# Kernel tuning notes

Measured on AMD Instinct MI355X. Metric: run time of the kernel, lower is better.

Reference implementation:

```python
import jax, jax.numpy as jnp
import numpy as np


def leaky(x):
    return jnp.where(x > 0, x, 0.2 * x)


def conv(x, w, b, s, p):
    y = jax.lax.conv_general_dilated(x, w, (s, s), [(p, p), (p, p)],
                                     dimension_numbers=('NCHW', 'OIHW', 'NCHW'))
    return y + b[None, :, None, None]


def maxpool2s1(x):
    return jax.lax.reduce_window(x, -jnp.inf, jax.lax.max, (1, 1, 2, 2), (1, 1, 1, 1), 'VALID')


def bn_eval(x, g, b, m, v):
    scale = g / jnp.sqrt(v + 1e-5)
    return (x - m[None, :, None, None]) * scale[None, :, None, None] + b[None, :, None, None]


def adaptive_avg_pool(x, oh, ow):
    # matches torch AdaptiveAvgPool2d window rule: [floor(i*H/o), ceil((i+1)*H/o))
    B, C, H, W = x.shape
    rows = []
    for i in range(oh):
        hs, he = (i * H) // oh, -((-(i + 1) * H) // oh)
        cols = []
        for j in range(ow):
            ws, we = (j * W) // ow, -((-(j + 1) * W) // ow)
            cols.append(x[:, :, hs:he, ws:we].mean((2, 3)))
        rows.append(jnp.stack(cols, -1))
    return jnp.stack(rows, -2)  # [B,C,oh,ow]


def forward(x, tw1, tb1, tw2, tb2, tw3, tb3, tw4, tb4,
            sw1, sb1, bn1_g, bn1_b, bn1_m, bn1_v,
            sw2, sb2, bn2_g, bn2_b, bn2_m, bn2_v,
            cw, cb, ew1, eb1, ew2, eb2, ew3, eb3):
    B = x.shape[0]
    E, K = ew1.shape[0], 2
    # --- scout router (BN in eval mode with running stats) ---
    h = jax.nn.relu(bn_eval(conv(x, sw1, sb1, 4, 3), bn1_g, bn1_b, bn1_m, bn1_v))
    h = jax.nn.relu(bn_eval(conv(h, sw2, sb2, 2, 1), bn2_g, bn2_b, bn2_m, bn2_v))
    logits = h.mean((2, 3)) @ cw.T + cb                       # [B,E]
    gate = jax.nn.softmax(logits, axis=-1)
    topk_p, topk_i = jax.lax.top_k(gate, K)                   # [B,K]
    topk_p = topk_p / (topk_p.sum(-1, keepdims=True) + 1e-6)
    # --- shared trunk ---
    t = maxpool2s1(leaky(conv(x, tw1, tb1, 4, 1)))            # 224->56->55
    t = maxpool2s1(leaky(conv(t, tw2, tb2, 2, 2)))            # 55->28->27
    t = leaky(conv(t, tw3, tb3, 1, 1))                        # 27
    t = maxpool2s1(leaky(conv(t, tw4, tb4, 1, 1)))            # 27->26
    t = adaptive_avg_pool(t, 3, 3)                            # [B,128,3,3]
    flat = t.reshape(B, -1)                                   # [B,1152]
    # --- MoE head: dense per-expert MLP, masked weighted combine ---
    h1 = leaky(jnp.einsum('bi,eoi->beo', flat, ew1) + eb1[None])   # [B,E,1024]
    h2 = leaky(jnp.einsum('beh,eoh->beo', h1, ew2) + eb2[None])    # [B,E,512]
    h3 = jnp.einsum('beh,eoh->beo', h2, ew3) + eb3[None]           # [B,E,feat]
    onehot = (topk_i[:, :, None] == jnp.arange(E)[None, None, :])  # [B,K,E]
    comb_w = jnp.sum(topk_p[:, :, None] * onehot, axis=1)          # [B,E]
    out = jnp.einsum('beo,be->bo', h3, comb_w)                     # [B,feat]
    return out


def setup_inputs() -> dict:
    key = jax.random.key(0)
    ks = jax.random.split(key, 32)
    W = 0.02
    d = {}
    d['x'] = jax.random.normal(ks[0], (256, 3, 224, 224), jnp.float32)
    d['tw1'] = jax.random.normal(ks[1], (16, 3, 3, 3), jnp.float32) * W
    d['tb1'] = jnp.zeros((16,), jnp.float32)
    d['tw2'] = jax.random.normal(ks[2], (32, 16, 5, 5), jnp.float32) * W
    d['tb2'] = jnp.zeros((32,), jnp.float32)
    d['tw3'] = jax.random.normal(ks[3], (64, 32, 3, 3), jnp.float32) * W
    d['tb3'] = jnp.zeros((64,), jnp.float32)
    d['tw4'] = jax.random.normal(ks[4], (128, 64, 3, 3), jnp.float32) * W
    d['tb4'] = jnp.zeros((128,), jnp.float32)
    d['sw1'] = jax.random.normal(ks[5], (16, 3, 7, 7), jnp.float32) * W
    d['sb1'] = jnp.zeros((16,), jnp.float32)
    d['bn1_g'] = jnp.ones((16,), jnp.float32)
    d['bn1_b'] = jnp.zeros((16,), jnp.float32)
    d['bn1_m'] = jnp.zeros((16,), jnp.float32)
    d['bn1_v'] = jnp.ones((16,), jnp.float32)
    d['sw2'] = jax.random.normal(ks[6], (32, 16, 3, 3), jnp.float32) * W
    d['sb2'] = jnp.zeros((32,), jnp.float32)
    d['bn2_g'] = jnp.ones((32,), jnp.float32)
    d['bn2_b'] = jnp.zeros((32,), jnp.float32)
    d['bn2_m'] = jnp.zeros((32,), jnp.float32)
    d['bn2_v'] = jnp.ones((32,), jnp.float32)
    d['cw'] = jax.random.normal(ks[7], (3, 32), jnp.float32) * W
    d['cb'] = jnp.zeros((3,), jnp.float32)
    d['ew1'] = jax.random.normal(ks[8], (3, 1024, 1152), jnp.float32) * W
    d['eb1'] = jnp.zeros((3, 1024), jnp.float32)
    d['ew2'] = jax.random.normal(ks[9], (3, 512, 1024), jnp.float32) * W
    d['eb2'] = jnp.zeros((3, 512), jnp.float32)
    d['ew3'] = jax.random.normal(ks[10], (3, 512, 512), jnp.float32) * W
    d['eb3'] = jnp.zeros((3, 512), jnp.float32)
    return d


def reference(x, tw1, tb1, tw2, tb2, tw3, tb3, tw4, tb4,
              sw1, sb1, bn1_g, bn1_b, bn1_m, bn1_v,
              sw2, sb2, bn2_g, bn2_b, bn2_m, bn2_v,
              cw, cb, ew1, eb1, ew2, eb2, ew3, eb3):
    return forward(x, tw1, tb1, tw2, tb2, tw3, tb3, tw4, tb4,
                   sw1, sb1, bn1_g, bn1_b, bn1_m, bn1_v,
                   sw2, sb2, bn2_g, bn2_b, bn2_m, bn2_v,
                   cw, cb, ew1, eb1, ew2, eb2, ew3, eb3)
```

## Files before the change

### kernel.cpp

```cpp
#include <hip/hip_runtime.h>

#define DEV static __device__ __forceinline__

constexpr int BATCH = 256;

DEV float leakyf(float x){ return x > 0.f ? x : 0.2f * x; }

typedef _Float16 f16x8 __attribute__((ext_vector_type(8)));
typedef float f32x4 __attribute__((ext_vector_type(4)));

DEV f16x8 max8(f16x8 a, f16x8 b){
  f16x8 r;
  #pragma unroll
  for (int j = 0; j < 8; ++j) r[j] = a[j] > b[j] ? a[j] : b[j];
  return r;
}

template<int IC,int OC>
DEV void wpackM_body(int i, const float* __restrict__ w, _Float16* __restrict__ wp){
  constexpr int F = OC/16;
  int j = i & 7, L = (i >> 3) & 63, rest = i >> 9;
  int f = rest % F; int q2 = rest / F; int s = q2 % (IC/32); int t = q2 / (IC/32);
  int oc = f*16 + (L & 15), ic = s*32 + (L >> 4)*8 + j;
  wp[i] = (_Float16)w[((size_t)oc*IC + ic)*9 + t];
}

template<int OC,int K>
DEV void wpackS_body(int i, const float* __restrict__ w, _Float16* __restrict__ wp){
  constexpr int F = OC/16, KWP = (K+1)/2;
  int j = i & 7, L = (i >> 3) & 63, rest = i >> 9;
  int f = rest % F, s = rest / F;
  int kh = s / KWP, kwp = s % KWP;
  int k = (L >> 4)*8 + j;
  int kw = 2*kwp + (k >> 4), ic = k & 15;
  int oc = f*16 + (L & 15);
  float v = (kw < K) ? w[((size_t)(oc*16 + ic)*K + kh)*K + kw] : 0.f;
  wp[i] = (_Float16)v;
}

DEV void wpackF_body(int i, const float* __restrict__ sw1,
                     const float* __restrict__ tw1, _Float16* __restrict__ wp){
  int j = i & 7, L = (i >> 3) & 63, rest = i >> 9;
  int nf = rest & 1, s = rest >> 1;
  int k = s*32 + (L >> 4)*8 + j;
  int oc = L & 15;
  int t = k / 48, c = k % 48;
  int dr = (t >> 1) - 1, dc = (t & 1) - 1;
  int ic = c >> 4, pr = (c >> 2) & 3, pc = c & 3;
  float v = 0.f;
  if (nf == 0){
    int kh = 4*dr + pr + 3, kw = 4*dc + pc + 3;
    if (kh >= 0 && kh < 7 && kw >= 0 && kw < 7) v = sw1[((oc*3 + ic)*7 + kh)*7 + kw];
  } else {
    int kh = 4*dr + pr + 1, kw = 4*dc + pc + 1;
    if (kh >= 0 && kh < 3 && kw >= 0 && kw < 3) v = tw1[((oc*3 + ic)*3 + kh)*3 + kw];
  }
  wp[i] = (_Float16)v;
}

template<int KTOT>
DEV void wpackG_body(int i, int e, const float* __restrict__ w, int N,
                     _Float16* __restrict__ wp){
  const int NF = N >> 4;
  const int total = NF * (KTOT >> 5) * 512;
  w  += (size_t)e * N * KTOT;
  wp += (size_t)e * total;
  int j = i & 7, L = (i >> 3) & 63, rest = i >> 9;
  int nf = rest % NF, t = rest / NF;
  int n = nf*16 + (L & 15), k = t*32 + (L >> 4)*8 + j;
  wp[i] = (_Float16)w[(size_t)n*KTOT + k];
}

__global__ __launch_bounds__(256) void wpackC_k(
    const float* __restrict__ tw3, _Float16* __restrict__ wpk3,
    const float* __restrict__ tw4, _Float16* __restrict__ wpk4,
    const float* __restrict__ tw2, _Float16* __restrict__ wp2,
    const float* __restrict__ sw2, _Float16* __restrict__ wps2,
    const float* __restrict__ sw1, const float* __restrict__ tw1,
    _Float16* __restrict__ wpf, float* __restrict__ gsum){
  const int b = blockIdx.x;
  const int tid = threadIdx.x;
  if (b < 72){
    wpackM_body<32,64>(b*256 + tid, tw3, wpk3);
  } else if (b < 360){
    wpackM_body<64,128>((b-72)*256 + tid, tw4, wpk4);
  } else if (b < 420){
    wpackS_body<32,5>((b-360)*256 + tid, tw2, wp2);
  } else if (b < 444){
    wpackS_body<32,3>((b-420)*256 + tid, sw2, wps2);
  } else if (b < 468){
    wpackF_body((b-444)*256 + tid, sw1, tw1, wpf);
  } else {
    gsum[(b-468)*256 + tid] = 0.f;
  }
}

__global__ __launch_bounds__(256) void fusedX_k(
    const float* __restrict__ x,
    const _Float16* __restrict__ W,
    const float* __restrict__ sb, const float* __restrict__ cb_,
    const float* __restrict__ g, const float* __restrict__ bt,
    const float* __restrict__ mn, const float* __restrict__ vr,
    _Float16* __restrict__ s1out, _Float16* __restrict__ c1out,
    const float* __restrict__ ew1, _Float16* __restrict__ ewp1,
    const float* __restrict__ ew2, _Float16* __restrict__ ewp2,
    const float* __restrict__ ew3, _Float16* __restrict__ ewp3){
  __shared__ __align__(16) _Float16 Ah[3*58*64];
  const int tid = threadIdx.x;
  const int b = blockIdx.x;

  if (b < 23040){
    if (b < 13824){
      wpackG_body<1152>((b % 4608)*256 + tid, b / 4608, ew1, 1024, ewp1);
    } else if (b < 19968){
      int t2 = b - 13824;
      wpackG_body<1024>((t2 % 2048)*256 + tid, t2 / 2048, ew2, 512, ewp2);
    } else {
      int t3 = b - 19968;
      wpackG_body<512>((t3 % 1024)*256 + tid, t3 / 1024, ew3, 512, ewp3);
    }
    return;
  }

  const int lb = b - 23040;
  const int w = (lb & 7)*896 + (lb >> 3);
  const int n = w / 28, oh0 = (w % 28) * 2;

  if (tid < 48){
    int rr = tid >> 4, side = (tid >> 3) & 1, q = tid & 7;
    int col = side ? 57 : 0;
    *(int4*)((char*)Ah + (((rr*58 + col) << 7) + q*16)) = (int4){0,0,0,0};
  }

  {
    const int m = tid & 63;
    const bool mok = (m < 56);
    const int mc = mok ? m : 55;
    const int cc = m + 1;
    const int rc0 = tid >> 6;

    float4 vv[9];
    {
      int ic   = (rc0 == 3) ? 0 : rc0;
      int ridx = (rc0 == 3) ? 1 : 0;
      #pragma unroll
      for (int j = 0; j < 9; ++j){
        const int ih = 4*oh0 - 4 + ridx;
        const int ihc = ih < 0 ? 0 : ih;
        const float* p = x + ((size_t)(n*3 + ic)*224 + ihc)*224 + 4*mc;
        asm volatile("global_load_dwordx4 %0, %1, off"
                     : "=v"(vv[j]) : "v"(p));
        ic += 1; ridx += 1;
        if (ic >= 3){ ic -= 3; ridx += 1; }
      }
    }
    asm volatile("s_waitcnt vmcnt(0)" ::: "memory");
    __builtin_amdgcn_sched_barrier(0);
    if (mok){
      int ic   = (rc0 == 3) ? 0 : rc0;
      int ridx = (rc0 == 3) ? 1 : 0;
      #pragma unroll
      for (int j = 0; j < 9; ++j){
        const int ih = 4*oh0 - 4 + ridx;
        float4 v = (ih >= 0) ? vv[j] : (float4){0.f,0.f,0.f,0.f};
        const int rr = ridx >> 2, pr = ridx & 3;
        int boff = (((rr*58 + cc) << 7) + ic*32 + pr*8) ^ ((cc & 7) << 4);
        _Float16 h4[4] = {(_Float16)v.x, (_Float16)v.y,
                          (_Float16)v.z, (_Float16)v.w};
        *(unsigned long long*)((char*)Ah + boff) = *(unsigned long long*)h4;
        ic += 1; ridx += 1;
        if (ic >= 3){ ic -= 3; ridx += 1; }
      }
    }
  }
  __syncthreads();

  const int wid = tid >> 6, lane = tid & 63;
  const int kg8 = (lane >> 4) * 8;
  f32x4 acc[2][2];
  #pragma unroll
  for (int mi = 0; mi < 2; ++mi)
    #pragma unroll
    for (int nf = 0; nf < 2; ++nf) acc[mi][nf] = (f32x4){0.f,0.f,0.f,0.f};

  #pragma unroll
  for (int s = 0; s < 6; ++s){
    const int kk = s*32 + kg8;
    const int t = kk / 48, c0 = kk - t*48;
    const int ra = t >> 1, ca = t & 1;
    f16x8 ah[2];
    #pragma unroll
    for (int mi = 0; mi < 2; ++mi){
      const int m = 2*wid + mi;
      const int rowsel = m >> 2;
      const int ow = (m & 3)*16 + (lane & 15);
      const int owc = ow > 55 ? 55 : ow;
      const int col = owc + ca;
      const int bidx = ((((rowsel + ra)*58 + col) << 7) + c0*2) ^ ((col & 7) << 4);
      ah[mi] = *(const f16x8*)((const char*)Ah + bidx);
    }
    #pragma unroll
    for (int nf = 0; nf < 2; ++nf){
      const f16x8 bw = *(const f16x8*)(W + (s*2 + nf)*512 + lane*8);
      #pragma unroll
      for (int mi = 0; mi < 2; ++mi)
        acc[mi][nf] = __builtin_amdgcn_mfma_f32_16x16x32_f16(ah[mi], bw, acc[mi][nf], 0,0,0);
    }
  }

  const int oc = lane & 15;
  const float sbv = sb[oc];
  const float scv = g[oc] * __frsqrt_rn(vr[oc] + 1e-5f);
  const float mnv = mn[oc], btv = bt[oc], cbv = cb_[oc];
  #pragma unroll
  for (int mi = 0; mi < 2; ++mi){
    const int m = 2*wid + mi;
    const int row = oh0 + (m >> 2);
    const int owb = (m & 3)*16 + (lane >> 4)*4;
    #pragma unroll
    for (int r = 0; r < 4; ++r){
      const int ow = owb + r;
      if (ow >= 56) continue;
      float vs = acc[mi][0][r] + sbv;
      vs = fmaxf((vs - mnv)*scv + btv, 0.f);
      const size_t o = (((size_t)n*56 + row)*56 + ow)*16 + oc;
      s1out[o] = (_Float16)vs;
      c1out[o] = (_Float16)leakyf(acc[mi][1][r] + cbv);
    }
  }
}

template<int OC,int K,int P,int IH,int IW,int ACT,bool OUT16,bool GATE,bool POOLIN>
DEV void convS_body(int bx, int tid, _Float16* A, float* gred,
    const _Float16* __restrict__ in,
    const _Float16* __restrict__ W,
    const float* __restrict__ bias,
    const float* __restrict__ bng, const float* __restrict__ bnb,
    const float* __restrict__ bnm, const float* __restrict__ bnv,
    float* __restrict__ outF, _Float16* __restrict__ outH,
    float* __restrict__ gsum){
  constexpr int F = OC/16, KWP = (K+1)/2;
  constexpr int RW = POOLIN ? (IW+1) : IW;

  const int n = bx / 28, oh = bx % 28;

  if (GATE && tid < 32) gred[tid] = 0.f;

  for (int i = tid; i < K*60*2; i += 256){
    int half = i & 1; int p = i >> 1;
    int c = p % 60; int r = p / 60;
    int ih = 2*oh - P + r, iw = c - P;
    int4 v = {0,0,0,0};
    if (ih >= 0 && ih < IH && iw >= 0 && iw < IW){
      const _Float16* q = in + (((size_t)n*(POOLIN ? IH+1 : IH) + ih)*RW + iw)*16 + half*8;
      if (POOLIN){
        f16x8 a = *(const f16x8*)q;
        f16x8 b = *(const f16x8*)(q + 16);
        f16x8 cc = *(const f16x8*)(q + RW*16);
        f16x8 d = *(const f16x8*)(q + RW*16 + 16);
        f16x8 mx = max8(max8(a, b), max8(cc, d));
        v = *(int4*)&mx;
      } else {
        v = *(const int4*)q;
      }
    }
    int byte = ((r*60 + c)*32 + half*16) ^ (((c>>1)&7) << 4);
    *(int4*)((char*)A + byte) = v;
  }
  __syncthreads();

  const int wid = tid >> 6, lane = tid & 63;
  const int fsel = wid & 1, mb = wid >> 1;
  const int ow_l = min(mb*16 + (lane & 15), 27);
  const int ic0b = ((lane >> 4) & 1) * 16;
  const int kwo  = (lane >> 4) >> 1;

  f32x4 acc = {0.f,0.f,0.f,0.f};
  #pragma unroll
  for (int kh = 0; kh < K; ++kh){
    #pragma unroll
    for (int kwp = 0; kwp < KWP; ++kwp){
      const int kw = 2*kwp + kwo;
      const int c = 2*ow_l + kw;
      int byte = ((kh*60 + c)*32 + ic0b) ^ (((c>>1)&7) << 4);
      f16x8 a = *(const f16x8*)((const char*)A + byte);
      const int s = kh*KWP + kwp;
      const f16x8 b = *(const f16x8*)(W + (s*F + fsel)*512 + lane*8);
      acc = __builtin_amdgcn_mfma_f32_16x16x32_f16(a, b, acc, 0,0,0);
    }
  }

  const int oc = fsel*16 + (lane & 15);
  float bv = bias[oc], sc = 1.f, mm = 0.f, bb = 0.f;
  if (ACT == 1){
    sc = bng[oc] * __frsqrt_rn(bnv[oc] + 1e-5f);
    mm = bnm[oc]; bb = bnb[oc];
  }
  float lsum = 0.f;
  #pragma unroll
  for (int r = 0; r < 4; ++r){
    const int ow = mb*16 + (lane >> 4)*4 + r;
    if (ow >= 28) continue;
    float v = acc[r] + bv;
    if (ACT == 1) v = fmaxf((v - mm)*sc + bb, 0.f);
    else          v = leakyf(v);
    if (GATE){
      lsum += v;
    } else {
      const size_t o = (((size_t)n*28 + oh)*28 + ow)*OC + oc;
      if (OUT16) outH[o] = (_Float16)v;
      else       outF[o] = v;
    }
  }
  if (GATE){
    atomicAdd(&gred[oc], lsum);
    __syncthreads();
    if (tid < 32) atomicAdd(&gsum[n*32 + tid], gred[tid]);
  }
}

__global__ __launch_bounds__(256) void convSS_k(
    const _Float16* __restrict__ s1h, const _Float16* __restrict__ wps2,
    const float* __restrict__ sb2,
    const float* __restrict__ bn2g, const float* __restrict__ bn2b,
    const float* __restrict__ bn2m, const float* __restrict__ bn2v,
    float* __restrict__ gsum,
    const _Float16* __restrict__ c1h, const _Float16* __restrict__ wp2,
    const float* __restrict__ tb2, _Float16* __restrict__ c2h){
  __shared__ __align__(16) _Float16 A[5*60*16];
  __shared__ float gred[32];
  const int tid = threadIdx.x;
  if (blockIdx.x < BATCH*28){
    convS_body<32,3,1,56,56,1,false,true,false>(blockIdx.x, tid, A, gred,
        s1h, wps2, sb2, bn2g, bn2b, bn2m, bn2v, nullptr, nullptr, gsum);
  } else {
    convS_body<32,5,2,55,55,0,true,false,true>(blockIdx.x - BATCH*28, tid, A, gred,
        c1h, wp2, tb2, nullptr, nullptr, nullptr, nullptr, nullptr, c2h, nullptr);
  }
}

template<int IC,int OC,bool POOLIN>
__global__ __launch_bounds__(256) void convM_k(
    const _Float16* __restrict__ Ag,
    const _Float16* __restrict__ W,
    const float* __restrict__ bias,
    _Float16* __restrict__ Out)
{
  constexpr int S = IC/32, FTOT = OC/16, FW = FTOT/2;
  constexpr int ICB = IC*2, ICG = ICB/16;
  __shared__ __align__(16) char A[4*34*ICB];

  const int tid = threadIdx.x;
  const int bx = blockIdx.x;
  const int n = bx / 14, pr = bx % 14;
  const int oh0 = pr * 2;

  for (int g = tid; g < 4*34*ICG; g += 256){
    int r = g / (34*ICG);
    int rem = g - r*(34*ICG);
    int c = rem / ICG, q = rem - c*ICG;
    int ir = oh0 + r - 1, icol = c - 1;
    int4 v = {0,0,0,0};
    if (ir >= 0 && ir < 27 && icol >= 0 && icol < 27){
      if (POOLIN){
        const _Float16* p0 = Ag + (((size_t)n*28 + ir)*28 + icol)*IC + q*8;
        f16x8 a = *(const f16x8*)p0;
        f16x8 b = *(const f16x8*)(p0 + IC);
        f16x8 cc = *(const f16x8*)(p0 + 28*IC);
        f16x8 d = *(const f16x8*)(p0 + 28*IC + IC);
        f16x8 mx = max8(max8(a, b), max8(cc, d));
        v = *(int4*)&mx;
      } else {
        v = *(const int4*)(Ag + (((size_t)n*27 + ir)*27 + icol)*IC + q*8);
      }
    }
    int off = (r*34 + c)*ICB + q*16;
    int swz = off ^ ((c & 7) << 4);
    *(int4*)(A + swz) = v;
  }
  __syncthreads();

  const int wid = tid >> 6, lane = tid & 63;
  const int rsel = wid & 1, ocq = wid >> 1;
  const int c0 = lane & 15, kg = (lane >> 4) * 16;
  const int colb0 = c0*ICB + kg, colb1 = (16 + c0)*ICB + kg;
  int msk[3];
  #pragma unroll
  for (int kw = 0; kw < 3; ++kw) msk[kw] = ((c0 + kw) & 7) << 4;

  f32x4 acc[2][FW];
  #pragma unroll
  for (int m = 0; m < 2; ++m)
    #pragma unroll
    for (int f = 0; f < FW; ++f) acc[m][f] = (f32x4){0.f,0.f,0.f,0.f};

  #pragma unroll
  for (int kh = 0; kh < 3; ++kh){
    #pragma unroll
    for (int kw = 0; kw < 3; ++kw){
      #pragma unroll
      for (int s = 0; s < S; ++s){
        const int fr0 = (((kh*3 + kw)*S + s)*FTOT + ocq*FW) * 512 + lane*8;
        f16x8 b[FW];
        #pragma unroll
        for (int f = 0; f < FW; ++f)
          b[f] = *(const f16x8*)(W + fr0 + f*512);
        const int base = ((rsel + kh)*34 + kw)*ICB + s*64;
        const int o0 = (base + colb0) ^ msk[kw];
        const int o1 = (base + colb1) ^ msk[kw];
        f16x8 a0 = *(const f16x8*)(A + o0);
        f16x8 a1 = *(const f16x8*)(A + o1);
        #pragma unroll
        for (int f = 0; f < FW; ++f){
          acc[0][f] = __builtin_amdgcn_mfma_f32_16x16x32_f16(a0, b[f], acc[0][f], 0,0,0);
          acc[1][f] = __builtin_amdgcn_mfma_f32_16x16x32_f16(a1, b[f], acc[1][f], 0,0,0);
        }
      }
    }
  }

  const int orow = oh0 + rsel;
  if (orow >= 27) return;
  #pragma unroll
  for (int f = 0; f < FW; ++f){
    const int oc = (ocq*FW + f)*16 + c0;
    const float bv = bias[oc];
    #pragma unroll
    for (int m = 0; m < 2; ++m){
      #pragma unroll
      for (int r = 0; r < 4; ++r){
        const int ow = m*16 + (lane >> 4)*4 + r;
        if (ow >= 27) continue;
        float v = leakyf(acc[m][f][r] + bv);
        Out[(((size_t)n*27 + orow)*27 + ow)*OC + oc] = (_Float16)v;
      }
    }
  }
}

template<int KTOT,int ACT>
__global__ __launch_bounds__(256) void gemmH_k(
    const _Float16* __restrict__ A, long strideA,
    const _Float16* __restrict__ W,
    const float* __restrict__ bias, int N,
    _Float16* __restrict__ OutH){
  const int e = blockIdx.z;
  A += (size_t)e * strideA;
  const int NF = N >> 4, KT = KTOT >> 5;
  W += (size_t)e * NF * KT * 512;
  const float* bs = bias + (size_t)e * N;
  const size_t ob = (size_t)e * 256 * N;

  const int tid = threadIdx.x, wid = tid >> 6, lane = tid & 63;
  const int mblk = blockIdx.x * 32;
  const int nf = blockIdx.y * 4 + wid;
  const int r0 = mblk + (lane & 15);
  const int kof = (lane >> 4) * 8;

  f32x4 acc0 = {0,0,0,0}, acc1 = {0,0,0,0};
  for (int t = 0; t < KT; ++t){
    const int k = t*32 + kof;
    f16x8 a0 = *(const f16x8*)(A + (size_t)r0*KTOT + k);
    f16x8 a1 = *(const f16x8*)(A + (size_t)(r0+16)*KTOT + k);
    const f16x8 b = *(const f16x8*)(W + ((size_t)t*NF + nf)*512 + lane*8);
    acc0 = __builtin_amdgcn_mfma_f32_16x16x32_f16(a0, b, acc0, 0,0,0);
    acc1 = __builtin_amdgcn_mfma_f32_16x16x32_f16(a1, b, acc1, 0,0,0);
  }
  const int n = nf*16 + (lane & 15);
  const float bv = bs[n];
  #pragma unroll
  for (int mi = 0; mi < 2; ++mi){
    f32x4 a = mi ? acc1 : acc0;
    #pragma unroll
    for (int r = 0; r < 4; ++r){
      const int m = mblk + mi*16 + (lane >> 4)*4 + r;
      float v = a[r] + bv;
      if (ACT == 1) v = leakyf(v);
      OutH[ob + (size_t)m*N + n] = (_Float16)v;
    }
  }
}

__global__ __launch_bounds__(256) void gemmC_k(
    const _Float16* __restrict__ A,
    const _Float16* __restrict__ W,
    const float* __restrict__ b3,
    const float* __restrict__ gsum,
    const float* __restrict__ cw, const float* __restrict__ cb,
    float* __restrict__ out){
  __shared__ float combL[16][3];
  const int tid = threadIdx.x, wid = tid >> 6, lane = tid & 63;
  const int mblk = blockIdx.x * 16;

  if (tid < 16){
    const int n = mblk + tid;
    float mch[32];
    #pragma unroll
    for (int c = 0; c < 32; ++c) mch[c] = gsum[n*32 + c] / 784.f;
    float lg[3];
    #pragma unroll
    for (int e = 0; e < 3; ++e){
      float a = cb[e];
      #pragma unroll
      for (int c = 0; c < 32; ++c) a += mch[c] * cw[e*32 + c];
      lg[e] = a;
    }
    float m = fmaxf(lg[0], fmaxf(lg[1], lg[2]));
    float ex[3], sum = 0.f;
    #pragma unroll
    for (int e = 0; e < 3; ++e){ ex[e] = expf(lg[e] - m); sum += ex[e]; }
    float pr[3];
    #pragma unroll
    for (int e = 0; e < 3; ++e) pr[e] = ex[e] / sum;
    int i1 = 0;
    if (pr[1] > pr[0]) i1 = 1;
    if (pr[2] > pr[i1]) i1 = 2;
    int i2 = -1;
    for (int e = 0; e < 3; ++e){
      if (e == i1) continue;
      if (i2 < 0 || pr[e] > pr[i2]) i2 = e;
    }
    float s12 = pr[i1] + pr[i2] + 1e-6f;
    float cmb[3] = {0.f, 0.f, 0.f};
    cmb[i1] = pr[i1] / s12;
    cmb[i2] = pr[i2] / s12;
    combL[tid][0] = cmb[0];
    combL[tid][1] = cmb[1];
    combL[tid][2] = cmb[2];
  }
  __syncthreads();

  const int nf = blockIdx.y * 4 + wid;
  const int r0 = mblk + (lane & 15);
  const int kof = (lane >> 4) * 8;
  const int n = nf*16 + (lane & 15);

  f32x4 oacc = {0.f,0.f,0.f,0.f};
  #pragma unroll
  for (int e = 0; e < 3; ++e){
    const _Float16* Ae = A + (size_t)e * 256 * 512;
    const _Float16* We = W + (size_t)e * 32 * 16 * 512;
    f32x4 acc = {0.f,0.f,0.f,0.f};
    for (int t = 0; t < 16; ++t){
      f16x8 a = *(const f16x8*)(Ae + (size_t)r0*512 + t*32 + kof);
      const f16x8 b = *(const f16x8*)(We + ((size_t)t*32 + nf)*512 + lane*8);
      acc = __builtin_amdgcn_mfma_f32_16x16x32_f16(a, b, acc, 0,0,0);
    }
    const float bv = b3[e*512 + n];
    #pragma unroll
    for (int r = 0; r < 4; ++r){
      const int lr = (lane >> 4)*4 + r;
      oacc[r] += combL[lr][e] * (acc[r] + bv);
    }
  }
  #pragma unroll
  for (int r = 0; r < 4; ++r){
    const int m = mblk + (lane >> 4)*4 + r;
    out[(size_t)m*512 + n] = oacc[r];
  }
}

__global__ __launch_bounds__(256) void papool2_k(const _Float16* __restrict__ in,
                                                 _Float16* __restrict__ flat16){
  __shared__ float red[2][128][9];
  const int n = blockIdx.x;
  const int tid = threadIdx.x;
  const int h = tid >> 7, c = tid & 127;
  const _Float16* p = in + (size_t)n * 729 * 128 + c;

  float sum[9];
  #pragma unroll
  for (int j = 0; j < 9; ++j) sum[j] = 0.f;

  float prev[27], cur[27];
  const int r0 = h * 13;
  #pragma unroll
  for (int rr = 0; rr < 14; ++rr){
    const int r = r0 + rr;
    #pragma unroll
    for (int cc = 0; cc < 27; ++cc)
      cur[cc] = (float)p[(size_t)(r*27 + cc) * 128];
    if (rr > 0){
      const int pr = r - 1;
      const bool b0 = (pr < 9), b1 = (pr >= 8) && (pr < 18), b2 = (pr >= 17);
      #pragma unroll
      for (int cc = 0; cc < 26; ++cc){
        float v = fmaxf(fmaxf(prev[cc], prev[cc+1]), fmaxf(cur[cc], cur[cc+1]));
        if (b0){
          if (cc < 9)             sum[0] += v;
          if (cc >= 8 && cc < 18) sum[1] += v;
          if (cc >= 17)           sum[2] += v;
        }
        if (b1){
          if (cc < 9)             sum[3] += v;
          if (cc >= 8 && cc < 18) sum[4] += v;
          if (cc >= 17)           sum[5] += v;
        }
        if (b2){
          if (cc < 9)             sum[6] += v;
          if (cc >= 8 && cc < 18) sum[7] += v;
          if (cc >= 17)           sum[8] += v;
        }
      }
    }
    #pragma unroll
    for (int cc = 0; cc < 27; ++cc) prev[cc] = cur[cc];
  }

  #pragma unroll
  for (int j = 0; j < 9; ++j) red[h][c][j] = sum[j];
  __syncthreads();

  if (tid < 128){
    const float rcp[9] = {1.f/81, 1.f/90, 1.f/81, 1.f/90, 1.f/100, 1.f/90,
                          1.f/81, 1.f/90, 1.f/81};
    _Float16* o = flat16 + (size_t)n * 1152 + tid * 9;
    #pragma unroll
    for (int j = 0; j < 9; ++j)
      o[j] = (_Float16)((red[0][tid][j] + red[1][tid][j]) * rcp[j]);
  }
}

extern "C" void kernel_launch(void* const* d_in, const int* in_sizes, int n_in,
                              void* d_out, int out_size, void* d_ws, size_t ws_size,
                              hipStream_t stream){
  const float* x    = (const float*)d_in[0];
  const float* tw1  = (const float*)d_in[1];  const float* tb1 = (const float*)d_in[2];
  const float* tw2  = (const float*)d_in[3];  const float* tb2 = (const float*)d_in[4];
  const float* tw3  = (const float*)d_in[5];  const float* tb3 = (const float*)d_in[6];
  const float* tw4  = (const float*)d_in[7];  const float* tb4 = (const float*)d_in[8];
  const float* sw1  = (const float*)d_in[9];  const float* sb1 = (const float*)d_in[10];
  const float* bn1g = (const float*)d_in[11]; const float* bn1b = (const float*)d_in[12];
  const float* bn1m = (const float*)d_in[13]; const float* bn1v = (const float*)d_in[14];
  const float* sw2  = (const float*)d_in[15]; const float* sb2 = (const float*)d_in[16];
  const float* bn2g = (const float*)d_in[17]; const float* bn2b = (const float*)d_in[18];
  const float* bn2m = (const float*)d_in[19]; const float* bn2v = (const float*)d_in[20];
  const float* cw   = (const float*)d_in[21]; const float* cb  = (const float*)d_in[22];
  const float* ew1  = (const float*)d_in[23]; const float* eb1 = (const float*)d_in[24];
  const float* ew2  = (const float*)d_in[25]; const float* eb2 = (const float*)d_in[26];
  const float* ew3  = (const float*)d_in[27]; const float* eb3 = (const float*)d_in[28];
  float* out = (float*)d_out;

  float* ws = (float*)d_ws;
  size_t off = 0;
  _Float16* flat16 = (_Float16*)(ws + off); off += 147456;
  float* gsum   = ws + off; off += BATCH * 32;
  _Float16* wpk3 = (_Float16*)(ws + off); off += 9216;
  _Float16* wpk4 = (_Float16*)(ws + off); off += 36864;
  _Float16* wp2  = (_Float16*)(ws + off); off += 7680;
  _Float16* wps2 = (_Float16*)(ws + off); off += 3072;
  _Float16* wpf  = (_Float16*)(ws + off); off += 3072;
  off += 16;
  float* bufA   = ws + off; off += 13778944;
  off += 16;
  float* bufB   = ws + off; off += 23887872;
  off += 16;
  (void)ws_size; (void)in_sizes; (void)n_in; (void)out_size;

  _Float16* s1h = (_Float16*)bufA;
  _Float16* C3u = (_Float16*)bufA;
  _Float16* ewp1 = (_Float16*)(bufA + 6500000);
  _Float16* ewp2 = ewp1 + 3538944;
  _Float16* ewp3 = ewp2 + 1572864;
  _Float16* c1h = (_Float16*)bufB;
  _Float16* c2h = (_Float16*)(bufB + 14000000);
  _Float16* c4h = (_Float16*)bufB;
  _Float16* h1  = (_Float16*)bufB;
  _Float16* h2  = h1 + 786432;

  dim3 blk(256);

  wpackC_k<<<dim3(500), blk, 0, stream>>>(
      tw3, wpk3, tw4, wpk4, tw2, wp2, sw2, wps2, sw1, tw1, wpf, gsum);

  fusedX_k<<<dim3(30208), blk, 0, stream>>>(
      x, wpf, sb1, tb1, bn1g, bn1b, bn1m, bn1v, s1h, c1h,
      ew1, ewp1, ew2, ewp2, ew3, ewp3);

  convSS_k<<<dim3(BATCH*28*2), blk, 0, stream>>>(
      s1h, wps2, sb2, bn2g, bn2b, bn2m, bn2v, gsum,
      c1h, wp2, tb2, c2h);

  convM_k<32,64,true><<<dim3(BATCH*14), blk, 0, stream>>>(
      c2h, wpk3, tb3, C3u);

  convM_k<64,128,false><<<dim3(BATCH*14), blk, 0, stream>>>(
      C3u, wpk4, tb4, c4h);

  papool2_k<<<dim3(BATCH), blk, 0, stream>>>(c4h, flat16);

  gemmH_k<1152,1><<<dim3(8,16,3), blk, 0, stream>>>(
      flat16, 0L, ewp1, eb1, 1024, h1);
  gemmH_k<1024,1><<<dim3(8,8,3), blk, 0, stream>>>(
      h1, 256L*1024, ewp2, eb2, 512, h2);
  gemmC_k<<<dim3(16,8), blk, 0, stream>>>(
      h2, ewp3, eb3, gsum, cw, cb, out);
}
```

Measured before the change: 244.7 us.

## Process four output rows per block in fused first conv with ring-buffered input

Each block of the fused first-layer conv now produces four output rows instead of two. It reuses the shared input row that overlaps between the two row pairs through a three-slot ring buffer in LDS. Loads for the second pair's new input rows are issued before the first pair's MFMA compute, which overlaps global latency with compute, and the conv grid shrinks by half. This cuts redundant input reads and per-block setup, at the cost of more registers held across compute, extra barriers, and fewer blocks for occupancy.

```diff
diff --git a/kernel.cpp b/kernel.cpp
--- a/kernel.cpp
+++ b/kernel.cpp
@@ -123,8 +123,8 @@
   }
 
   const int lb = b - 23040;
-  const int w = (lb & 7)*896 + (lb >> 3);
-  const int n = w / 28, oh0 = (w % 28) * 2;
+  const int w = (lb & 7)*448 + (lb >> 3);
+  const int n = w / 14, oh0 = (w % 14) * 4;
 
   if (tid < 48){
     int rr = tid >> 4, side = (tid >> 3) & 1, q = tid & 7;
@@ -132,13 +132,13 @@
     *(int4*)((char*)Ah + (((rr*58 + col) << 7) + q*16)) = (int4){0,0,0,0};
   }
 
+  const int m = tid & 63;
+  const bool mok = (m < 56);
+  const int mc = mok ? m : 55;
+  const int cc = m + 1;
+  const int rc0 = tid >> 6;
+
   {
-    const int m = tid & 63;
-    const bool mok = (m < 56);
-    const int mc = mok ? m : 55;
-    const int cc = m + 1;
-    const int rc0 = tid >> 6;
-
     float4 vv[9];
     {
       int ic   = (rc0 == 3) ? 0 : rc0;
@@ -175,59 +175,100 @@
   }
   __syncthreads();
 
+  float4 uu[6];
+  #pragma unroll
+  for (int j2 = 0; j2 < 6; ++j2){
+    const int k = rc0*6 + j2;
+    const int icn = k >> 3, nr = k & 7;
+    const int rrl = 1 + (nr >> 2), prn = nr & 3;
+    const int ih = 4*(oh0 + 1 + rrl) + prn;
+    const float* p = x + ((size_t)(n*3 + icn)*224 + ih)*224 + 4*mc;
+    asm volatile("global_load_dwordx4 %0, %1, off"
+                 : "=v"(uu[j2]) : "v"(p));
+  }
+
   const int wid = tid >> 6, lane = tid & 63;
   const int kg8 = (lane >> 4) * 8;
-  f32x4 acc[2][2];
-  #pragma unroll
-  for (int mi = 0; mi < 2; ++mi)
-    #pragma unroll
-    for (int nf = 0; nf < 2; ++nf) acc[mi][nf] = (f32x4){0.f,0.f,0.f,0.f};
-
-  #pragma unroll
-  for (int s = 0; s < 6; ++s){
-    const int kk = s*32 + kg8;
-    const int t = kk / 48, c0 = kk - t*48;
-    const int ra = t >> 1, ca = t & 1;
-    f16x8 ah[2];
-    #pragma unroll
-    for (int mi = 0; mi < 2; ++mi){
-      const int m = 2*wid + mi;
-      const int rowsel = m >> 2;
-      const int ow = (m & 3)*16 + (lane & 15);
-      const int owc = ow > 55 ? 55 : ow;
-      const int col = owc + ca;
-      const int bidx = ((((rowsel + ra)*58 + col) << 7) + c0*2) ^ ((col & 7) << 4);
-      ah[mi] = *(const f16x8*)((const char*)Ah + bidx);
-    }
-    #pragma unroll
-    for (int nf = 0; nf < 2; ++nf){
-      const f16x8 bw = *(const f16x8*)(W + (s*2 + nf)*512 + lane*8);
-      #pragma unroll
-      for (int mi = 0; mi < 2; ++mi)
-        acc[mi][nf] = __builtin_amdgcn_mfma_f32_16x16x32_f16(ah[mi], bw, acc[mi][nf], 0,0,0);
-    }
-  }
-
   const int oc = lane & 15;
   const float sbv = sb[oc];
   const float scv = g[oc] * __frsqrt_rn(vr[oc] + 1e-5f);
   const float mnv = mn[oc], btv = bt[oc], cbv = cb_[oc];
-  #pragma unroll
-  for (int mi = 0; mi < 2; ++mi){
-    const int m = 2*wid + mi;
-    const int row = oh0 + (m >> 2);
-    const int owb = (m & 3)*16 + (lane >> 4)*4;
-    #pragma unroll
-    for (int r = 0; r < 4; ++r){
-      const int ow = owb + r;
-      if (ow >= 56) continue;
-      float vs = acc[mi][0][r] + sbv;
-      vs = fmaxf((vs - mnv)*scv + btv, 0.f);
-      const size_t o = (((size_t)n*56 + row)*56 + ow)*16 + oc;
-      s1out[o] = (_Float16)vs;
-      c1out[o] = (_Float16)leakyf(acc[mi][1][r] + cbv);
-    }
-  }
+
+  f32x4 acc[2][2];
+
+  auto comp = [&](int rbase){
+    #pragma unroll
+    for (int mi = 0; mi < 2; ++mi)
+      #pragma unroll
+      for (int nf = 0; nf < 2; ++nf) acc[mi][nf] = (f32x4){0.f,0.f,0.f,0.f};
+    #pragma unroll
+    for (int s = 0; s < 6; ++s){
+      const int kk = s*32 + kg8;
+      const int t = kk / 48, c0 = kk - t*48;
+      const int ra = t >> 1, ca = t & 1;
+      f16x8 ah[2];
+      #pragma unroll
+      for (int mi = 0; mi < 2; ++mi){
+        const int mm = 2*wid + mi;
+        const int rowsel = mm >> 2;
+        const int ow = (mm & 3)*16 + (lane & 15);
+        const int owc = ow > 55 ? 55 : ow;
+        const int col = owc + ca;
+        int phys = rowsel + ra + rbase;
+        if (phys >= 3) phys -= 3;
+        const int bidx = (((phys*58 + col) << 7) + c0*2) ^ ((col & 7) << 4);
+        ah[mi] = *(const f16x8*)((const char*)Ah + bidx);
+      }
+      #pragma unroll
+      for (int nf = 0; nf < 2; ++nf){
+        const f16x8 bw = *(const f16x8*)(W + (s*2 + nf)*512 + lane*8);
+        #pragma unroll
+        for (int mi = 0; mi < 2; ++mi)
+          acc[mi][nf] = __builtin_amdgcn_mfma_f32_16x16x32_f16(ah[mi], bw, acc[mi][nf], 0,0,0);
+      }
+    }
+  };
+
+  auto epi = [&](int rbase){
+    #pragma unroll
+    for (int mi = 0; mi < 2; ++mi){
+      const int mm = 2*wid + mi;
+      const int row = oh0 + rbase + (mm >> 2);
+      const int owb = (mm & 3)*16 + (lane >> 4)*4;
+      #pragma unroll
+      for (int r = 0; r < 4; ++r){
+        const int ow = owb + r;
+        if (ow >= 56) continue;
+        float vs = acc[mi][0][r] + sbv;
+        vs = fmaxf((vs - mnv)*scv + btv, 0.f);
+        const size_t o = (((size_t)n*56 + row)*56 + ow)*16 + oc;
+        s1out[o] = (_Float16)vs;
+        c1out[o] = (_Float16)leakyf(acc[mi][1][r] + cbv);
+      }
+    }
+  };
+
+  comp(0);
+  __syncthreads();
+  asm volatile("s_waitcnt vmcnt(0)" ::: "memory");
+  __builtin_amdgcn_sched_barrier(0);
+  if (mok){
+    #pragma unroll
+    for (int j2 = 0; j2 < 6; ++j2){
+      const int k = rc0*6 + j2;
+      const int icn = k >> 3, nr = k & 7;
+      const int rrp = nr >> 2, prn = nr & 3;
+      int boff = (((rrp*58 + cc) << 7) + icn*32 + prn*8) ^ ((cc & 7) << 4);
+      _Float16 h4[4] = {(_Float16)uu[j2].x, (_Float16)uu[j2].y,
+                        (_Float16)uu[j2].z, (_Float16)uu[j2].w};
+      *(unsigned long long*)((char*)Ah + boff) = *(unsigned long long*)h4;
+    }
+  }
+  epi(0);
+  __syncthreads();
+
+  comp(2);
+  epi(2);
 }
 
 template<int OC,int K,int P,int IH,int IW,int ACT,bool OUT16,bool GATE,bool POOLIN>
@@ -673,7 +714,7 @@
   wpackC_k<<<dim3(500), blk, 0, stream>>>(
       tw3, wpk3, tw4, wpk4, tw2, wp2, sw2, wps2, sw1, tw1, wpf, gsum);
 
-  fusedX_k<<<dim3(30208), blk, 0, stream>>>(
+  fusedX_k<<<dim3(26624), blk, 0, stream>>>(
       x, wpf, sb1, tb1, bn1g, bn1b, bn1m, bn1v, s1h, c1h,
       ew1, ewp1, ew2, ewp2, ew3, ewp3);
 
```

Measured after the change: 247.0 us. About the same (+0.9%).
